# Performance work log

Measured on AMD Instinct MI355X. Metric: run time of the kernel, lower is better.

## Reference

```python
import jax, jax.numpy as jnp
import numpy as np

EMBED_DIM = 1024
NUM_HEADS = 16
HEAD_DIM = EMBED_DIM // NUM_HEADS
ROPE_BASE = 10000.0


def rotate_half(x):
    # interleaved variant: pairs (x0,x1) -> (-x1, x0)
    x1 = x[..., ::2]
    x2 = x[..., 1::2]
    return jnp.stack((-x2, x1), axis=-1).reshape(x.shape)


def rope_tables(T, dim, dtype):
    inv_freq = 1.0 / (ROPE_BASE ** (jnp.arange(0, dim, 2, dtype=jnp.float32) / dim))
    t = jnp.arange(T, dtype=jnp.float32)
    freqs = t[:, None] * inv_freq[None, :]          # [T, dim/2]
    emb = jnp.concatenate((freqs, freqs), axis=-1)  # [T, dim]
    return jnp.cos(emb).astype(dtype), jnp.sin(emb).astype(dtype)


def setup_inputs() -> dict:
    key = jax.random.key(0)
    kx, kq, ko = jax.random.split(key, 3)
    B, T, D = 2, 2048, EMBED_DIM
    x = jax.random.normal(kx, (B, T, D), dtype=jnp.float32)
    s = 1.0 / np.sqrt(D)
    Wqkv = jax.random.normal(kq, (D, 3 * D), dtype=jnp.float32) * s
    Wout = jax.random.normal(ko, (D, D), dtype=jnp.float32) * s
    return {"x": x, "Wqkv": Wqkv, "Wout": Wout}


def reference(x, Wqkv, Wout):
    B, T, D = x.shape
    H, hd = NUM_HEADS, HEAD_DIM
    qkv = x @ Wqkv                                   # [B,T,3D]
    q, k, v = jnp.split(qkv, 3, axis=-1)
    q = q.reshape(B, T, H, hd).transpose(0, 2, 1, 3)  # [B,H,T,hd]
    k = k.reshape(B, T, H, hd).transpose(0, 2, 1, 3)
    v = v.reshape(B, T, H, hd).transpose(0, 2, 1, 3)
    cos, sin = rope_tables(T, hd, x.dtype)           # [T,hd]
    cos = cos[None, None, :, :]
    sin = sin[None, None, :, :]
    q = q * cos + rotate_half(q) * sin
    k = k * cos + rotate_half(k) * sin
    scale = 1.0 / np.sqrt(hd).astype(np.float32)
    attn = jnp.einsum('bhtd,bhsd->bhts', q, k) * scale  # [B,H,T,T]
    attn = jax.nn.softmax(attn, axis=-1)
    out = jnp.einsum('bhts,bhsd->bhtd', attn, v)     # [B,H,T,hd]
    out = out.transpose(0, 2, 1, 3).reshape(B, T, D)
    return out @ Wout
```

## Files before the change

### kernel.cpp

```cpp
#include <hip/hip_runtime.h>
#include <hip/hip_bf16.h>
#include <stdint.h>


typedef unsigned short u16;
typedef short bf16x8 __attribute__((ext_vector_type(8)));
typedef float f32x4  __attribute__((ext_vector_type(4)));

#if defined(__has_builtin) && __has_builtin(__builtin_amdgcn_exp2f)
#define EXP2F(x) __builtin_amdgcn_exp2f(x)
#else
#define EXP2F(x) exp2f(x)
#endif

__device__ __forceinline__ u16 f2b(float f) {
  uint32_t u = __float_as_uint(f);
  u += 0x7fffu + ((u >> 16) & 1u);
  return (u16)(u >> 16);
}
__device__ __forceinline__ uint32_t pkbf(float a, float b) {
  __hip_bfloat162 h = __float22bfloat162_rn(make_float2(a, b));
  union { __hip_bfloat162 h2; uint32_t u; } cv; cv.h2 = h;
  return cv.u;
}

__device__ __forceinline__ void gl2lds16(const void* g, void* l) {
  __builtin_amdgcn_global_load_lds(
      (const __attribute__((address_space(1))) unsigned int*)g,
      (__attribute__((address_space(3))) unsigned int*)l, 16, 0, 0);
}

__global__ void sniff_kernel(const u16* x, int* flag) {
  __shared__ int cnt;
  if (threadIdx.x == 0) cnt = 0;
  __syncthreads();
  int c = 0;
  for (int i = threadIdx.x; i < 4096; i += 256) {
    float a = fabsf(__uint_as_float(((uint32_t)x[2*i]) << 16));
    if (a > 1e-3f && a < 100.f) c++;
  }
  atomicAdd(&cnt, c);
  __syncthreads();
  if (threadIdx.x == 0) *flag = (cnt > 2048) ? 1 : 0;
}

__device__ __forceinline__ void tr_tile(const void* src, u16* dst, int Kd, int N,
                                        int n0, int k0, int isb, u16* Lt, int tid)
{
  const int r = tid >> 2, cseg = (tid & 3) << 4;
  u16 t[16];
  if (isb) {
    const u16* s = (const u16*)src + (size_t)(k0 + r) * N + n0 + cseg;
    *(uint4*)&t[0] = *(const uint4*)s;
    *(uint4*)&t[8] = *(const uint4*)(s + 8);
  } else {
    const float* s = (const float*)src + (size_t)(k0 + r) * N + n0 + cseg;
    #pragma unroll
    for (int j = 0; j < 4; j++) {
      float4 v = *(const float4*)(s + j * 4);
      t[j*4+0] = f2b(v.x); t[j*4+1] = f2b(v.y); t[j*4+2] = f2b(v.z); t[j*4+3] = f2b(v.w);
    }
  }
  #pragma unroll
  for (int j = 0; j < 16; j++) Lt[(cseg + j) * 72 + r] = t[j];
  __syncthreads();
  const int n = tid >> 2, kseg = (tid & 3) << 4;
  uint4 u0 = *(const uint4*)&Lt[n * 72 + kseg];
  uint4 u1 = *(const uint4*)&Lt[n * 72 + kseg + 8];
  u16* d = dst + (size_t)(n0 + n) * Kd + k0 + kseg;
  *(uint4*)d = u0;
  *(uint4*)(d + 8) = u1;
}

__global__ __launch_bounds__(256) void prep_kernel(
    const void* __restrict__ x, const void* __restrict__ wqkv,
    const void* __restrict__ wout, const int* __restrict__ flag,
    u16* __restrict__ Xb, u16* __restrict__ Wqkvt, u16* __restrict__ Woutt,
    float2* __restrict__ CS)
{
  __shared__ u16 Lt[64 * 72];
  const int isb = *flag;
  const int bid = blockIdx.x, tid = threadIdx.x;
  if (bid < 2048) {
    const size_t i = ((size_t)bid * 256 + tid) * 8;
    if (isb) {
      *(uint4*)&Xb[i] = *(const uint4*)((const u16*)x + i);
    } else {
      const float* s = (const float*)x + i;
      float4 a = *(const float4*)s, b = *(const float4*)(s + 4);
      uint4 p;
      p.x = pkbf(a.x, a.y); p.y = pkbf(a.z, a.w);
      p.z = pkbf(b.x, b.y); p.w = pkbf(b.z, b.w);
      *(uint4*)&Xb[i] = p;
    }
  } else if (bid < 2816) {
    const int b = bid - 2048;
    tr_tile(wqkv, Wqkvt, 1024, 3072, (b % 48) * 64, (b / 48) * 64, isb, Lt, tid);
  } else if (bid < 3072) {
    const int b = bid - 2816;
    tr_tile(wout, Woutt, 1024, 1024, (b % 16) * 64, (b / 16) * 64, isb, Lt, tid);
  } else {
    const int idx = (bid - 3072) * 256 + tid;
    const int t = idx >> 5, f = idx & 31;
    float invf = __expf(-(float)f * 0.2878231366242557f);
    float th = (float)t * invf;
    float sn, cs;
    sincosf(th, &sn, &cs);
    CS[idx] = make_float2(cs, sn);
  }
}

__global__ __launch_bounds__(256) void qkv_kernel(
    const u16* __restrict__ Xb, const u16* __restrict__ Wt,
    const float2* __restrict__ CS,
    u16* __restrict__ Q, u16* __restrict__ K, u16* __restrict__ Vt)
{
  __shared__ u16 As[128 * 64];
  __shared__ u16 Bs[128 * 64];
  const int tid = threadIdx.x;
  const int n0 = blockIdx.x * 128;
  const int m0 = blockIdx.y * 128;
  const int w = tid >> 6, l = tid & 63, lr = l & 15, lq = l >> 4;
  const int mrow0 = (w & 1) * 64;
  const int ncol0 = (w >> 1) * 64;
  const int srow = tid >> 3;
  const int gseg = (tid & 7) ^ (srow & 7);

  const int col0 = n0 + ncol0;
  const int sec = col0 >> 10;
  const int isv = (sec == 2);
  const int h = (col0 >> 6) & 15;

  f32x4 acc[4][4] = {};

  for (int k0 = 0; k0 < 1024; k0 += 64) {
    __syncthreads();
    #pragma unroll
    for (int rd = 0; rd < 4; rd++) {
      const int row = srow + rd * 32;
      gl2lds16(Xb + (size_t)(m0 + row) * 1024 + k0 + gseg * 8, &As[tid * 8 + rd * 2048]);
      gl2lds16(Wt + (size_t)(n0 + row) * 1024 + k0 + gseg * 8, &Bs[tid * 8 + rd * 2048]);
    }
    __syncthreads();
    #pragma unroll
    for (int kc = 0; kc < 2; kc++) {
      bf16x8 af[4], bf[4];
      #pragma unroll
      for (int i = 0; i < 4; i++) {
        const int seg = ((kc << 2) | lq) ^ (lr & 7);
        af[i] = *(const bf16x8*)&As[(mrow0 + i * 16 + lr) * 64 + seg * 8];
        bf[i] = *(const bf16x8*)&Bs[(ncol0 + i * 16 + lr) * 64 + seg * 8];
      }
      if (isv) {
        #pragma unroll
        for (int mb = 0; mb < 4; mb++)
          #pragma unroll
          for (int nb = 0; nb < 4; nb++)
            acc[mb][nb] = __builtin_amdgcn_mfma_f32_16x16x32_bf16(af[mb], bf[nb], acc[mb][nb], 0, 0, 0);
      } else {
        #pragma unroll
        for (int mb = 0; mb < 4; mb++)
          #pragma unroll
          for (int nb = 0; nb < 4; nb++)
            acc[mb][nb] = __builtin_amdgcn_mfma_f32_16x16x32_bf16(bf[nb], af[mb], acc[mb][nb], 0, 0, 0);
      }
    }
  }

  if (isv) {
    #pragma unroll
    for (int mb = 0; mb < 4; mb++) {
      const int row0 = m0 + mrow0 + mb * 16 + lq * 4;
      const int b = row0 >> 11, t0 = row0 & 2047;
      const int tp = (t0 & ~31) | (((t0 >> 2) & 3) << 3) | (((t0 >> 4) & 1) << 2);
      #pragma unroll
      for (int nb = 0; nb < 4; nb++) {
        const int d = nb * 16 + lr;
        uint2 uv;
        uv.x = pkbf(acc[mb][nb][0], acc[mb][nb][1]);
        uv.y = pkbf(acc[mb][nb][2], acc[mb][nb][3]);
        *(uint2*)&Vt[(((size_t)b * 16 + h) * 64 + d) * 2048 + tp] = uv;
      }
    }
  } else {
    u16* dst = (sec == 0) ? Q : K;
    const float qscale = 0.125f * 1.44269504f;
    #pragma unroll
    for (int mb = 0; mb < 4; mb++) {
      const int m = m0 + mrow0 + mb * 16 + lr;
      const int b = m >> 11, t = m & 2047;
      const float* csrow = (const float*)(CS + t * 32);
      #pragma unroll
      for (int nb = 0; nb < 4; nb++) {
        const int d = nb * 16 + lq * 4;
        const int fb = d & 31;
        f32x4 c01 = *(const f32x4*)(csrow + 2 * fb);
        f32x4 c23 = *(const f32x4*)(csrow + 2 * fb + 4);
        float v0 = acc[mb][nb][0], v1 = acc[mb][nb][1];
        float v2 = acc[mb][nb][2], v3 = acc[mb][nb][3];
        float r0 = v0 * c01[0] - v1 * c01[1];
        float r1 = fmaf(v1, c01[2], v0 * c01[3]);
        float r2 = v2 * c23[0] - v3 * c23[1];
        float r3 = fmaf(v3, c23[2], v2 * c23[3]);
        if (sec == 0) { r0 *= qscale; r1 *= qscale; r2 *= qscale; r3 *= qscale; }
        uint2 uv;
        uv.x = pkbf(r0, r1);
        uv.y = pkbf(r2, r3);
        *(uint2*)&dst[(((size_t)b * 16 + h) * 2048 + t) * 64 + d] = uv;
      }
    }
  }
}

__global__ __launch_bounds__(256, 4) void attn_kernel(
    const u16* __restrict__ Q, const u16* __restrict__ K,
    const u16* __restrict__ Vt, u16* __restrict__ ATT,
    float* __restrict__ Op, float* __restrict__ Ls, int ns)
{
  __shared__ u16 Ks[2][64 * 64];
  __shared__ u16 Vs[2][64 * 64];
  const int tid = threadIdx.x;
  const int w = tid >> 6, l = tid & 63, lr = l & 15, lq = l >> 4;

  const int nwg = 512 * ns;
  const int bid = blockIdx.x;
  const int swz = (bid & 7) * (nwg >> 3) + (bid >> 3);
  const int per_bh = 16 * ns;
  const int bh = swz / per_bh;
  const int rem = swz - bh * per_bh;
  const int sh = rem & (ns - 1);
  const int qt = rem / ns;

  const int slen = 2048 / ns;
  const int sbeg = sh * slen;
  const size_t base = (size_t)bh * (2048 * 64);
  const int qrow0 = qt * 128 + w * 32;

  bf16x8 qf[2][2];
  #pragma unroll
  for (int mb = 0; mb < 2; mb++)
    #pragma unroll
    for (int kc = 0; kc < 2; kc++)
      qf[mb][kc] = *(const bf16x8*)(Q + base + (size_t)(qrow0 + mb * 16 + lr) * 64 + kc * 32 + lq * 8);

  f32x4 oa[4][2] = {};
  float lsum[2] = {0.f, 0.f};

  const int srow = tid >> 3;

  auto stage = [&](int buf, int s0) {
    #pragma unroll
    for (int rd = 0; rd < 2; rd++) {
      const int row = srow + rd * 32;
      const int gs = (tid & 7) ^ (row & 7);
      gl2lds16(K + base + (size_t)(s0 + row) * 64 + gs * 8, &Ks[buf][tid * 8 + rd * 2048]);
      gl2lds16(Vt + base + (size_t)row * 2048 + s0 + gs * 8, &Vs[buf][tid * 8 + rd * 2048]);
    }
  };

  stage(0, sbeg);
  const int nt = slen >> 6;

  #pragma unroll 1
  for (int t = 0; t < nt; t++) {
    const int buf = t & 1;
    __syncthreads();
    if (t + 1 < nt) stage(buf ^ 1, sbeg + (t + 1) * 64);

    bf16x8 kf[4][2];
    #pragma unroll
    for (int sb = 0; sb < 4; sb++)
      #pragma unroll
      for (int kc = 0; kc < 2; kc++) {
        const int seg = ((kc << 2) | lq) ^ (lr & 7);
        kf[sb][kc] = *(const bf16x8*)&Ks[buf][(sb * 16 + lr) * 64 + seg * 8];
      }

    uint32_t pw[2][8];
    #pragma unroll
    for (int mb = 0; mb < 2; mb++) {
      f32x4 st[4];
      __builtin_amdgcn_s_setprio(1);
      #pragma unroll
      for (int sb = 0; sb < 4; sb++) {
        f32x4 z = {};
        z = __builtin_amdgcn_mfma_f32_16x16x32_bf16(kf[sb][0], qf[mb][0], z, 0, 0, 0);
        st[sb] = __builtin_amdgcn_mfma_f32_16x16x32_bf16(kf[sb][1], qf[mb][1], z, 0, 0, 0);
      }
      __builtin_amdgcn_s_setprio(0);
      #pragma unroll
      for (int sb = 0; sb < 4; sb++) {
        float e0 = EXP2F(st[sb][0]), e1 = EXP2F(st[sb][1]);
        float e2 = EXP2F(st[sb][2]), e3 = EXP2F(st[sb][3]);
        lsum[mb] += (e0 + e1) + (e2 + e3);
        pw[mb][2 * sb]     = pkbf(e0, e1);
        pw[mb][2 * sb + 1] = pkbf(e2, e3);
      }
    }

    bf16x8 vf[4][2];
    #pragma unroll
    for (int db = 0; db < 4; db++)
      #pragma unroll
      for (int kc = 0; kc < 2; kc++) {
        const int seg = ((kc << 2) | lq) ^ (lr & 7);
        vf[db][kc] = *(const bf16x8*)&Vs[buf][(db * 16 + lr) * 64 + seg * 8];
      }

    __builtin_amdgcn_s_setprio(1);
    #pragma unroll
    for (int mb = 0; mb < 2; mb++) {
      union { uint32_t u[4]; bf16x8 v; } p0, p1;
      p0.u[0] = pw[mb][0]; p0.u[1] = pw[mb][1]; p0.u[2] = pw[mb][2]; p0.u[3] = pw[mb][3];
      p1.u[0] = pw[mb][4]; p1.u[1] = pw[mb][5]; p1.u[2] = pw[mb][6]; p1.u[3] = pw[mb][7];
      #pragma unroll
      for (int db = 0; db < 4; db++) {
        oa[db][mb] = __builtin_amdgcn_mfma_f32_16x16x32_bf16(vf[db][0], p0.v, oa[db][mb], 0, 0, 0);
        oa[db][mb] = __builtin_amdgcn_mfma_f32_16x16x32_bf16(vf[db][1], p1.v, oa[db][mb], 0, 0, 0);
      }
    }
    __builtin_amdgcn_s_setprio(0);
  }

  #pragma unroll
  for (int mb = 0; mb < 2; mb++) {
    float v = lsum[mb];
    v += __shfl_xor(v, 16, 64);
    v += __shfl_xor(v, 32, 64);
    lsum[mb] = v;
  }

  const int b = bh >> 4, h = bh & 15;
  if (ns == 1) {
    #pragma unroll
    for (int mb = 0; mb < 2; mb++) {
      const float inv = 1.f / lsum[mb];
      const int t = qrow0 + mb * 16 + lr;
      u16* dst = ATT + ((size_t)(b * 2048 + t)) * 1024 + h * 64;
      #pragma unroll
      for (int db = 0; db < 4; db++) {
        uint2 u;
        u.x = pkbf(oa[db][mb][0] * inv, oa[db][mb][1] * inv);
        u.y = pkbf(oa[db][mb][2] * inv, oa[db][mb][3] * inv);
        *(uint2*)&dst[db * 16 + lq * 4] = u;
      }
    }
  } else {
    float* op = Op + (size_t)sh * (65536ull * 64);
    #pragma unroll
    for (int mb = 0; mb < 2; mb++) {
      const size_t row = (size_t)bh * 2048 + qrow0 + mb * 16 + lr;
      #pragma unroll
      for (int db = 0; db < 4; db++)
        *(f32x4*)&op[row * 64 + db * 16 + lq * 4] = oa[db][mb];
      if (lq == 0) Ls[(size_t)sh * 65536 + row] = lsum[mb];
    }
  }
}

__global__ __launch_bounds__(256) void combine_kernel(
    const float* __restrict__ Op, const float* __restrict__ Ls, u16* __restrict__ ATT)
{
  const int idx = blockIdx.x * 256 + threadIdx.x;
  const int R = idx >> 3;
  const int c = (idx & 7) * 8;
  const float* p0 = Op + (size_t)R * 64 + c;
  const float* p1 = p0 + 65536ull * 64;
  f32x4 a0 = *(const f32x4*)p0, a1 = *(const f32x4*)(p0 + 4);
  f32x4 b0 = *(const f32x4*)p1, b1 = *(const f32x4*)(p1 + 4);
  const float inv = 1.f / (Ls[R] + Ls[65536 + R]);
  const int bh = R >> 11, trow = R & 2047;
  const int b = bh >> 4, h = bh & 15;
  u16* d = ATT + ((size_t)(b * 2048 + trow)) * 1024 + h * 64 + c;
  uint4 u;
  u.x = pkbf((a0[0] + b0[0]) * inv, (a0[1] + b0[1]) * inv);
  u.y = pkbf((a0[2] + b0[2]) * inv, (a0[3] + b0[3]) * inv);
  u.z = pkbf((a1[0] + b1[0]) * inv, (a1[1] + b1[1]) * inv);
  u.w = pkbf((a1[2] + b1[2]) * inv, (a1[3] + b1[3]) * inv);
  *(uint4*)d = u;
}

__global__ __launch_bounds__(256) void outproj_kernel(
    const u16* __restrict__ A, const u16* __restrict__ Wt,
    const int* __restrict__ flag, void* __restrict__ outv)
{
  __shared__ u16 As[128 * 64];
  __shared__ u16 Bs[128 * 64];
  const int isb = *flag;
  const int tid = threadIdx.x;
  const int n0 = blockIdx.x * 128;
  const int m0 = blockIdx.y * 128;
  const int w = tid >> 6, l = tid & 63, lr = l & 15, lq = l >> 4;
  const int mrow0 = (w & 1) * 64;
  const int ncol0 = (w >> 1) * 64;
  const int srow = tid >> 3;
  const int gseg = (tid & 7) ^ (srow & 7);

  f32x4 acc[4][4] = {};

  for (int k0 = 0; k0 < 1024; k0 += 64) {
    __syncthreads();
    #pragma unroll
    for (int rd = 0; rd < 4; rd++) {
      const int row = srow + rd * 32;
      gl2lds16(A + (size_t)(m0 + row) * 1024 + k0 + gseg * 8, &As[tid * 8 + rd * 2048]);
      gl2lds16(Wt + (size_t)(n0 + row) * 1024 + k0 + gseg * 8, &Bs[tid * 8 + rd * 2048]);
    }
    __syncthreads();
    #pragma unroll
    for (int kc = 0; kc < 2; kc++) {
      bf16x8 af[4], bf[4];
      #pragma unroll
      for (int i = 0; i < 4; i++) {
        const int seg = ((kc << 2) | lq) ^ (lr & 7);
        af[i] = *(const bf16x8*)&As[(mrow0 + i * 16 + lr) * 64 + seg * 8];
        bf[i] = *(const bf16x8*)&Bs[(ncol0 + i * 16 + lr) * 64 + seg * 8];
      }
      #pragma unroll
      for (int mb = 0; mb < 4; mb++)
        #pragma unroll
        for (int nb = 0; nb < 4; nb++)
          acc[mb][nb] = __builtin_amdgcn_mfma_f32_16x16x32_bf16(bf[nb], af[mb], acc[mb][nb], 0, 0, 0);
    }
  }
  #pragma unroll
  for (int mb = 0; mb < 4; mb++) {
    const int row = m0 + mrow0 + mb * 16 + lr;
    #pragma unroll
    for (int nb = 0; nb < 4; nb++) {
      const int col = n0 + ncol0 + nb * 16 + lq * 4;
      f32x4 v = acc[mb][nb];
      if (isb) {
        uint2 uv;
        uv.x = pkbf(v[0], v[1]);
        uv.y = pkbf(v[2], v[3]);
        *(uint2*)&((u16*)outv)[(size_t)row * 1024 + col] = uv;
      } else {
        *(f32x4*)&((float*)outv)[(size_t)row * 1024 + col] = v;
      }
    }
  }
}

extern "C" void kernel_launch(void* const* d_in, const int* in_sizes, int n_in,
                              void* d_out, int out_size, void* d_ws, size_t ws_size,
                              hipStream_t stream)
{
  const void* x    = d_in[0];
  const void* wqkv = d_in[1];
  const void* wout = d_in[2];
  char* ws = (char*)d_ws;
  const size_t MB = 1024 * 1024;
  int*    flag   = (int*)ws;
  float2* CS     = (float2*)(ws + 1024);
  u16*    Xb     = (u16*)(ws + 1 * MB);
  u16*    ATT    = Xb;
  u16*    Wqkvt  = (u16*)(ws + 9 * MB);
  u16*    Woutt  = (u16*)(ws + 15 * MB);
  u16*    Q      = (u16*)(ws + 17 * MB);
  u16*    K      = (u16*)(ws + 25 * MB);
  u16*    Vt     = (u16*)(ws + 33 * MB);
  float*  Op     = (float*)(ws + 41 * MB);
  float*  Ls     = (float*)(ws + 75 * MB);

  const bool split = ws_size >= 76 * MB;
  const int ns = split ? 2 : 1;

  sniff_kernel<<<1, 256, 0, stream>>>((const u16*)x, flag);
  prep_kernel<<<3328, 256, 0, stream>>>(x, wqkv, wout, flag, Xb, Wqkvt, Woutt, CS);
  qkv_kernel<<<dim3(24, 32), 256, 0, stream>>>(Xb, Wqkvt, CS, Q, K, Vt);
  attn_kernel<<<dim3(512 * ns), 256, 0, stream>>>(Q, K, Vt, ATT, Op, Ls, ns);
  if (split)
    combine_kernel<<<2048, 256, 0, stream>>>(Op, Ls, ATT);
  outproj_kernel<<<dim3(8, 32), 256, 0, stream>>>(ATT, Woutt, flag, d_out);
}
```

Measured before the change: 208.8 us.

## Switch attention inner loops to 32x32x16 MFMA with matching V layout

Rewrites the attention kernel's QK^T and PV products to use 32x32x16 bf16 MFMA tiles instead of 16x16x32. Each lane now owns one query row, which cuts the row-sum reduction to a single shuffle. The V-transpose permutation written by the projection kernel and the LDS swizzle are changed to match the new fragment layout. The aim is fewer MFMA instructions per tile, fewer LDS fragment loads, and fewer bank conflicts. The cost is larger accumulator vectors per lane and changed register pressure.

```diff
diff --git a/kernel.cpp b/kernel.cpp
--- a/kernel.cpp
+++ b/kernel.cpp
@@ -6,6 +6,7 @@
 typedef unsigned short u16;
 typedef short bf16x8 __attribute__((ext_vector_type(8)));
 typedef float f32x4  __attribute__((ext_vector_type(4)));
+typedef float f32x16 __attribute__((ext_vector_type(16)));
 
 #if defined(__has_builtin) && __has_builtin(__builtin_amdgcn_exp2f)
 #define EXP2F(x) __builtin_amdgcn_exp2f(x)
@@ -172,7 +173,7 @@
     for (int mb = 0; mb < 4; mb++) {
       const int row0 = m0 + mrow0 + mb * 16 + lq * 4;
       const int b = row0 >> 11, t0 = row0 & 2047;
-      const int tp = (t0 & ~31) | (((t0 >> 2) & 3) << 3) | (((t0 >> 4) & 1) << 2);
+      const int tp = (t0 & ~12) | ((t0 & 4) << 1) | ((t0 & 8) >> 1);
       #pragma unroll
       for (int nb = 0; nb < 4; nb++) {
         const int d = nb * 16 + lr;
@@ -220,7 +221,8 @@
   __shared__ u16 Ks[2][64 * 64];
   __shared__ u16 Vs[2][64 * 64];
   const int tid = threadIdx.x;
-  const int w = tid >> 6, l = tid & 63, lr = l & 15, lq = l >> 4;
+  const int w = tid >> 6, l = tid & 63;
+  const int m5 = l & 31, hi = l >> 5;
 
   const int nwg = 512 * ns;
   const int bid = blockIdx.x;
@@ -235,16 +237,15 @@
   const int sbeg = sh * slen;
   const size_t base = (size_t)bh * (2048 * 64);
   const int qrow0 = qt * 128 + w * 32;
-
-  bf16x8 qf[2][2];
+  const int t_own = qrow0 + m5;
+
+  bf16x8 qf[4];
   #pragma unroll
-  for (int mb = 0; mb < 2; mb++)
-    #pragma unroll
-    for (int kc = 0; kc < 2; kc++)
-      qf[mb][kc] = *(const bf16x8*)(Q + base + (size_t)(qrow0 + mb * 16 + lr) * 64 + kc * 32 + lq * 8);
-
-  f32x4 oa[4][2] = {};
-  float lsum[2] = {0.f, 0.f};
+  for (int kd = 0; kd < 4; kd++)
+    qf[kd] = *(const bf16x8*)(Q + base + (size_t)t_own * 64 + kd * 16 + hi * 8);
+
+  f32x16 oa[2] = {};
+  float lsum = 0.f;
 
   const int srow = tid >> 3;
 
@@ -252,7 +253,7 @@
     #pragma unroll
     for (int rd = 0; rd < 2; rd++) {
       const int row = srow + rd * 32;
-      const int gs = (tid & 7) ^ (row & 7);
+      const int gs = (tid & 7) ^ (row & 7) ^ ((row >> 3) & 3);
       gl2lds16(K + base + (size_t)(s0 + row) * 64 + gs * 8, &Ks[buf][tid * 8 + rd * 2048]);
       gl2lds16(Vt + base + (size_t)row * 2048 + s0 + gs * 8, &Vs[buf][tid * 8 + rd * 2048]);
     }
@@ -267,94 +268,83 @@
     __syncthreads();
     if (t + 1 < nt) stage(buf ^ 1, sbeg + (t + 1) * 64);
 
-    bf16x8 kf[4][2];
-    #pragma unroll
-    for (int sb = 0; sb < 4; sb++)
-      #pragma unroll
-      for (int kc = 0; kc < 2; kc++) {
-        const int seg = ((kc << 2) | lq) ^ (lr & 7);
-        kf[sb][kc] = *(const bf16x8*)&Ks[buf][(sb * 16 + lr) * 64 + seg * 8];
-      }
-
     uint32_t pw[2][8];
     #pragma unroll
-    for (int mb = 0; mb < 2; mb++) {
-      f32x4 st[4];
+    for (int sb = 0; sb < 2; sb++) {
+      const int row = sb * 32 + m5;
+      const int sw = (row & 7) ^ ((row >> 3) & 3);
+      bf16x8 kf[4];
+      #pragma unroll
+      for (int kd = 0; kd < 4; kd++)
+        kf[kd] = *(const bf16x8*)&Ks[buf][row * 64 + ((((kd << 1) | hi) ^ sw) << 3)];
+      f32x16 z = {};
       __builtin_amdgcn_s_setprio(1);
-      #pragma unroll
-      for (int sb = 0; sb < 4; sb++) {
-        f32x4 z = {};
-        z = __builtin_amdgcn_mfma_f32_16x16x32_bf16(kf[sb][0], qf[mb][0], z, 0, 0, 0);
-        st[sb] = __builtin_amdgcn_mfma_f32_16x16x32_bf16(kf[sb][1], qf[mb][1], z, 0, 0, 0);
-      }
+      z = __builtin_amdgcn_mfma_f32_32x32x16_bf16(kf[0], qf[0], z, 0, 0, 0);
+      z = __builtin_amdgcn_mfma_f32_32x32x16_bf16(kf[1], qf[1], z, 0, 0, 0);
+      z = __builtin_amdgcn_mfma_f32_32x32x16_bf16(kf[2], qf[2], z, 0, 0, 0);
+      z = __builtin_amdgcn_mfma_f32_32x32x16_bf16(kf[3], qf[3], z, 0, 0, 0);
       __builtin_amdgcn_s_setprio(0);
-      #pragma unroll
-      for (int sb = 0; sb < 4; sb++) {
-        float e0 = EXP2F(st[sb][0]), e1 = EXP2F(st[sb][1]);
-        float e2 = EXP2F(st[sb][2]), e3 = EXP2F(st[sb][3]);
-        lsum[mb] += (e0 + e1) + (e2 + e3);
-        pw[mb][2 * sb]     = pkbf(e0, e1);
-        pw[mb][2 * sb + 1] = pkbf(e2, e3);
-      }
-    }
-
-    bf16x8 vf[4][2];
-    #pragma unroll
-    for (int db = 0; db < 4; db++)
-      #pragma unroll
-      for (int kc = 0; kc < 2; kc++) {
-        const int seg = ((kc << 2) | lq) ^ (lr & 7);
-        vf[db][kc] = *(const bf16x8*)&Vs[buf][(db * 16 + lr) * 64 + seg * 8];
-      }
-
-    __builtin_amdgcn_s_setprio(1);
-    #pragma unroll
-    for (int mb = 0; mb < 2; mb++) {
-      union { uint32_t u[4]; bf16x8 v; } p0, p1;
-      p0.u[0] = pw[mb][0]; p0.u[1] = pw[mb][1]; p0.u[2] = pw[mb][2]; p0.u[3] = pw[mb][3];
-      p1.u[0] = pw[mb][4]; p1.u[1] = pw[mb][5]; p1.u[2] = pw[mb][6]; p1.u[3] = pw[mb][7];
-      #pragma unroll
-      for (int db = 0; db < 4; db++) {
-        oa[db][mb] = __builtin_amdgcn_mfma_f32_16x16x32_bf16(vf[db][0], p0.v, oa[db][mb], 0, 0, 0);
-        oa[db][mb] = __builtin_amdgcn_mfma_f32_16x16x32_bf16(vf[db][1], p1.v, oa[db][mb], 0, 0, 0);
-      }
-    }
-    __builtin_amdgcn_s_setprio(0);
-  }
-
-  #pragma unroll
-  for (int mb = 0; mb < 2; mb++) {
-    float v = lsum[mb];
-    v += __shfl_xor(v, 16, 64);
-    v += __shfl_xor(v, 32, 64);
-    lsum[mb] = v;
-  }
+      float e[16];
+      #pragma unroll
+      for (int r = 0; r < 16; r++) e[r] = EXP2F(z[r]);
+      lsum += (((e[0] + e[1]) + (e[2] + e[3])) + ((e[4] + e[5]) + (e[6] + e[7])))
+            + (((e[8] + e[9]) + (e[10] + e[11])) + ((e[12] + e[13]) + (e[14] + e[15])));
+      #pragma unroll
+      for (int w2 = 0; w2 < 8; w2++)
+        pw[sb][w2] = pkbf(e[2 * w2], e[2 * w2 + 1]);
+    }
+
+    #pragma unroll
+    for (int db = 0; db < 2; db++) {
+      const int row = db * 32 + m5;
+      const int sw = (row & 7) ^ ((row >> 3) & 3);
+      bf16x8 vf[4];
+      #pragma unroll
+      for (int sblk = 0; sblk < 4; sblk++)
+        vf[sblk] = *(const bf16x8*)&Vs[buf][row * 64 + ((((sblk << 1) | hi) ^ sw) << 3)];
+      __builtin_amdgcn_s_setprio(1);
+      #pragma unroll
+      for (int sblk = 0; sblk < 4; sblk++) {
+        union { uint32_t u[4]; bf16x8 v; } pf;
+        const int sb = sblk >> 1, off = (sblk & 1) * 4;
+        pf.u[0] = pw[sb][off + 0]; pf.u[1] = pw[sb][off + 1];
+        pf.u[2] = pw[sb][off + 2]; pf.u[3] = pw[sb][off + 3];
+        oa[db] = __builtin_amdgcn_mfma_f32_32x32x16_bf16(vf[sblk], pf.v, oa[db], 0, 0, 0);
+      }
+      __builtin_amdgcn_s_setprio(0);
+    }
+  }
+
+  lsum += __shfl_xor(lsum, 32, 64);
 
   const int b = bh >> 4, h = bh & 15;
   if (ns == 1) {
-    #pragma unroll
-    for (int mb = 0; mb < 2; mb++) {
-      const float inv = 1.f / lsum[mb];
-      const int t = qrow0 + mb * 16 + lr;
-      u16* dst = ATT + ((size_t)(b * 2048 + t)) * 1024 + h * 64;
-      #pragma unroll
-      for (int db = 0; db < 4; db++) {
+    const float inv = 1.f / lsum;
+    u16* dst = ATT + ((size_t)(b * 2048 + t_own)) * 1024 + h * 64;
+    #pragma unroll
+    for (int db = 0; db < 2; db++)
+      #pragma unroll
+      for (int rq = 0; rq < 4; rq++) {
+        const int d0 = db * 32 + rq * 8 + hi * 4;
         uint2 u;
-        u.x = pkbf(oa[db][mb][0] * inv, oa[db][mb][1] * inv);
-        u.y = pkbf(oa[db][mb][2] * inv, oa[db][mb][3] * inv);
-        *(uint2*)&dst[db * 16 + lq * 4] = u;
-      }
-    }
+        u.x = pkbf(oa[db][4 * rq + 0] * inv, oa[db][4 * rq + 1] * inv);
+        u.y = pkbf(oa[db][4 * rq + 2] * inv, oa[db][4 * rq + 3] * inv);
+        *(uint2*)&dst[d0] = u;
+      }
   } else {
     float* op = Op + (size_t)sh * (65536ull * 64);
-    #pragma unroll
-    for (int mb = 0; mb < 2; mb++) {
-      const size_t row = (size_t)bh * 2048 + qrow0 + mb * 16 + lr;
-      #pragma unroll
-      for (int db = 0; db < 4; db++)
-        *(f32x4*)&op[row * 64 + db * 16 + lq * 4] = oa[db][mb];
-      if (lq == 0) Ls[(size_t)sh * 65536 + row] = lsum[mb];
-    }
+    const size_t row = (size_t)bh * 2048 + t_own;
+    #pragma unroll
+    for (int db = 0; db < 2; db++)
+      #pragma unroll
+      for (int rq = 0; rq < 4; rq++) {
+        const int d0 = db * 32 + rq * 8 + hi * 4;
+        f32x4 v;
+        v[0] = oa[db][4 * rq + 0]; v[1] = oa[db][4 * rq + 1];
+        v[2] = oa[db][4 * rq + 2]; v[3] = oa[db][4 * rq + 3];
+        *(f32x4*)&op[row * 64 + d0] = v;
+      }
+    if (hi == 0) Ls[(size_t)sh * 65536 + row] = lsum;
   }
 }
 
```

After: 209.5 us. No clear change (+0.4%).
